# Performance work log

Hardware: AMD Instinct MI355X
Metric: run time of the kernel (lower is better)

Reference implementation:

```python
import jax, jax.numpy as jnp
from jax import lax
import numpy as np

B, P, C = 16, 21824, 2          # batch, num_priors, num_classes
KCAND = 1024                    # candidate cap for jittable NMS
TOP_K = 750
CONF_THRESH = 0.3
IOU_THRESH = 0.01
VAR = (0.1, 0.2)
IMG_SCALE = 1024.0


def setup_inputs() -> dict:
    key = jax.random.key(0)
    k1, k2, k3 = jax.random.split(key, 3)
    return {
        "boxes_logits": jax.random.normal(k1, (B, P, 4), dtype=jnp.float32),
        "cls_logits": jax.random.normal(k2, (B, P, C), dtype=jnp.float32),
        "priors": jax.random.uniform(k3, (P, 4), dtype=jnp.float32),
    }


def decode(loc, priors):
    # priors are (cx, cy, w, h); loc are SSD-style offsets
    xy = priors[..., :2] + loc[..., :2] * VAR[0] * priors[..., 2:]
    wh = priors[..., 2:] * jnp.exp(loc[..., 2:] * VAR[1])
    x1y1 = xy - wh * 0.5
    x2y2 = x1y1 + wh
    return jnp.concatenate([x1y1, x2y2], axis=-1) * IMG_SCALE


def iou_matrix(b):
    # b: [K,4] in x1y1x2y2; torchvision-style IoU (areas unclamped, inter clamped)
    area = (b[:, 2] - b[:, 0]) * (b[:, 3] - b[:, 1])
    lt = jnp.maximum(b[:, None, :2], b[None, :, :2])
    rb = jnp.minimum(b[:, None, 2:], b[None, :, 2:])
    wh = jnp.clip(rb - lt, 0.0)
    inter = wh[..., 0] * wh[..., 1]
    union = area[:, None] + area[None, :] - inter
    return inter / jnp.maximum(union, 1e-9)


def greedy_nms(iou, valid, thresh):
    # boxes assumed sorted by descending score; returns keep mask [K]
    K = iou.shape[0]
    iou = jnp.where(jnp.eye(K, dtype=bool), 0.0, iou)  # ignore self-overlap

    def step(suppressed, i):
        keep_i = jnp.logical_and(~suppressed[i], valid[i])
        suppressed = jnp.logical_or(suppressed, keep_i & (iou[i] > thresh))
        return suppressed, keep_i

    _, keep = lax.scan(step, jnp.zeros(K, dtype=bool), jnp.arange(K))
    return keep


def _detect_one(boxes, scores_all):
    # boxes [P,4], scores_all [P,C]
    scores = scores_all[:, 1:].reshape(-1)                        # drop background
    labels = jnp.broadcast_to(jnp.arange(1, C), (P, C - 1)).reshape(-1)
    bx = jnp.broadcast_to(boxes[:, None, :], (P, C - 1, 4)).reshape(-1, 4)

    masked = jnp.where(scores > CONF_THRESH, scores, -1.0)
    top_scores, idx = lax.top_k(masked, KCAND)                    # score-sorted candidates
    cb = bx[idx]                                                  # [K,4]
    cl = labels[idx]                                              # [K]
    valid = top_scores > CONF_THRESH

    # batched_nms: offset boxes per class so classes never overlap
    max_c = jnp.max(jnp.where(valid[:, None], cb, 0.0))
    off = cl.astype(cb.dtype)[:, None] * (max_c + 1.0)
    keep = greedy_nms(iou_matrix(cb + off), valid, IOU_THRESH)

    kept_scores = jnp.where(keep, top_scores, -1.0)
    final_s, kidx = lax.top_k(kept_scores, TOP_K)                 # keep[:top_k] in score order
    mask = keep[kidx]
    out_boxes = jnp.where(mask[:, None], cb[kidx], 0.0)
    out_scores = jnp.where(mask, final_s, 0.0)
    out_labels = jnp.where(mask, cl[kidx], 0)
    return out_boxes, out_scores, out_labels, mask


def reference(boxes_logits, cls_logits, priors):
    scores_logits = jax.nn.softmax(cls_logits, axis=2)            # [B,P,C]
    boxes = decode(boxes_logits, priors)                          # [B,P,4]
    pred_boxes, pred_scores, pred_labels, mask = jax.vmap(_detect_one)(boxes, scores_logits)
    return pred_boxes, pred_scores, pred_labels, mask
```

## Files before the change

### kernel.cpp

```cpp
#include <hip/hip_runtime.h>

typedef unsigned long long u64;
typedef unsigned int u32;

#define KC 1024
#define TOPK 750
#define CONF 0.3f
#define IOU_T 0.01f
#define WINB 0x2F80u
#define NW 128
#define CCAP 2048

__device__ __forceinline__ u64 score_key(const float* __restrict__ c2, u32 p) {
    float a0 = c2[0], a1 = c2[1];
    float m  = fmaxf(a0, a1);
    float e0 = expf(a0 - m), e1 = expf(a1 - m);
    float s  = e1 / (e0 + e1);
    float ms = s > CONF ? s : -1.0f;
    u32 u = __float_as_uint(ms);
    u32 mapped = (u & 0x80000000u) ? ~u : (u | 0x80000000u);
    return ((u64)mapped << 32) | (u32)(~p);
}

__device__ __forceinline__ void decode_key(u64 key, int b, int tid,
        const float* __restrict__ bl, const float* __restrict__ priors, int P,
        float& x1, float& y1, float& x2, float& y2, float& score, bool& valid) {
    u32 mapped = (u32)(key >> 32);
    u32 fb = (mapped & 0x80000000u) ? (mapped & 0x7fffffffu) : ~mapped;
    float s = __uint_as_float(fb);
    u32 p = ~(u32)(key & 0xffffffffull);
    if (key == 0ull) { s = -1.0f; p = (u32)tid; }
    score = s; valid = (s > CONF);
    const float* pr4 = priors + (size_t)p * 4;
    const float* lc  = bl + ((size_t)b * P + p) * 4;
    float pcx = pr4[0], pcy = pr4[1], pw = pr4[2], ph = pr4[3];
    float lx = lc[0], ly = lc[1], lw = lc[2], lh = lc[3];
    float cx = pcx + lx * 0.1f * pw;
    float cy = pcy + ly * 0.1f * ph;
    float w  = pw * expf(lw * 0.2f);
    float h  = ph * expf(lh * 0.2f);
    float t1x = cx - w * 0.5f;
    float t1y = cy - h * 0.5f;
    x1 = t1x * 1024.0f;
    y1 = t1y * 1024.0f;
    x2 = (t1x + w) * 1024.0f;
    y2 = (t1y + h) * 1024.0f;
}

__global__ __launch_bounds__(1024) void k_hist(const float* __restrict__ cls,
                                               u32* __restrict__ hist, int P) {
    __shared__ u32 lh[NW];
    int t = threadIdx.x;
    if (t < NW) lh[t] = 0;
    __syncthreads();
    int p = blockIdx.x * 1024 + t;
    int b = blockIdx.y;
    if (p < P) {
        u64 k = score_key(cls + ((size_t)b * P + p) * 2, (u32)p);
        u32 wbin = (u32)(k >> 50) - WINB;
        if (wbin < (u32)NW) atomicAdd(&lh[wbin], 1u);
    }
    __syncthreads();
    if (t < NW) { u32 c = lh[t]; if (c) atomicAdd(&hist[(size_t)b * NW + t], c); }
}

__global__ __launch_bounds__(256) void k_compact(const float* __restrict__ cls,
        const u32* __restrict__ hist, u32* __restrict__ sufx, u32* __restrict__ tot,
        u32* __restrict__ bfill, u64* __restrict__ cbuf2, int P) {
    int b = blockIdx.y, t = threadIdx.x;
    __shared__ u32 sh[NW], sa[NW], sb_[NW];
    __shared__ int sh_cut;
    if (t == 0) sh_cut = 0;
    if (t < NW) { u32 h = hist[(size_t)b * NW + t]; sh[t] = h; sa[t] = h; }
    __syncthreads();
    u32 *src = sa, *dst = sb_;
    for (int d = 1; d < NW; d <<= 1) {
        if (t < NW) dst[t] = src[t] + ((t + d < NW) ? src[t + d] : 0u);
        __syncthreads();
        u32* tmp = src; src = dst; dst = tmp;
    }
    if (t < NW && src[t] >= KC) atomicMax(&sh_cut, t);
    __syncthreads();
    int cutw = sh_cut;
    if (blockIdx.x == 0) {
        if (t < NW) sufx[(size_t)b * NW + t] = src[t] - sh[t];
        if (t == 0) tot[b] = src[cutw];
    }
    int p = blockIdx.x * 256 + t;
    if (p < P) {
        u64 k = score_key(cls + ((size_t)b * P + p) * 2, (u32)p);
        u32 wbin = (u32)(k >> 50) - WINB;
        if (wbin < (u32)NW && (int)wbin >= cutw) {
            u32 pos = (src[wbin] - sh[wbin]) + atomicAdd(&bfill[(size_t)b * NW + wbin], 1u);
            if (pos < CCAP) cbuf2[(size_t)b * CCAP + pos] = k;
        }
    }
}

__global__ void k_rank(const u64* __restrict__ cbuf2, const u32* __restrict__ hist,
                       const u32* __restrict__ sufx, const u32* __restrict__ tot,
                       u64* __restrict__ csorted) {
    int b = blockIdx.y;
    u32 s = blockIdx.x * 64 + threadIdx.x;
    u32 T = tot[b]; if (T > CCAP) T = CCAP;
    if (s >= T) return;
    const u64* cb = cbuf2 + (size_t)b * CCAP;
    u64 key = cb[s];
    u32 w = (u32)(key >> 50) - WINB;
    u32 seg0 = sufx[(size_t)b * NW + w];
    u32 segN = seg0 + hist[(size_t)b * NW + w];
    if (segN > T) segN = T;
    u32 cnt = 0;
    for (u32 j = seg0; j < segN; ++j) cnt += (cb[j] > key) ? 1u : 0u;
    u32 r = seg0 + cnt;
    if (r < KC) csorted[(size_t)b * KC + r] = key;
}

__global__ __launch_bounds__(1024) void k_iou(const u64* __restrict__ csorted,
        const float* __restrict__ bl, const float* __restrict__ priors,
        u64* __restrict__ rows, int P) {
    int b = blockIdx.y, tid = threadIdx.x;
    int rowbase = blockIdx.x * 16;
    __shared__ float sx1[KC], sy1[KC], sx2[KC], sy2[KC], sar[KC];
    __shared__ float smax[KC];
    float x1, y1, x2, y2, score; bool valid;
    decode_key(csorted[(size_t)b * KC + tid], b, tid, bl, priors, P,
               x1, y1, x2, y2, score, valid);
    smax[tid] = valid ? fmaxf(fmaxf(x1, y1), fmaxf(x2, y2)) : 0.0f;
    __syncthreads();
    for (int st = 512; st > 0; st >>= 1) {
        if (tid < st) smax[tid] = fmaxf(smax[tid], smax[tid + st]);
        __syncthreads();
    }
    float off = smax[0] + 1.0f;
    float xs1 = x1 + off, ys1 = y1 + off, xs2 = x2 + off, ys2 = y2 + off;
    sx1[tid] = xs1; sy1[tid] = ys1; sx2[tid] = xs2; sy2[tid] = ys2;
    sar[tid] = (xs2 - xs1) * (ys2 - ys1);
    __syncthreads();

    int w = tid >> 6, lane = tid & 63;
    int r = rowbase + w;
    float rx1 = sx1[r], ry1 = sy1[r], rx2 = sx2[r], ry2 = sy2[r], rar = sar[r];
    u64* rb = rows + ((size_t)b * KC + r) * 16;
    #pragma unroll 4
    for (int c = 0; c < 16; ++c) {
        int col = c * 64 + lane;
        float ltx = fmaxf(rx1, sx1[col]), lty = fmaxf(ry1, sy1[col]);
        float rbx = fminf(rx2, sx2[col]), rby = fminf(ry2, sy2[col]);
        float ww = fmaxf(rbx - ltx, 0.0f), hh = fmaxf(rby - lty, 0.0f);
        float inter = ww * hh;
        float uni = rar + sar[col] - inter;
        float iou = inter / fmaxf(uni, 1e-9f);
        bool pred = (iou > IOU_T) && (col != r);
        u64 m = __ballot(pred);
        if (lane == 0) rb[c] = m;
    }
}

__global__ __launch_bounds__(1024) void k_scan(const u64* __restrict__ csorted,
        const u64* __restrict__ rows, const float* __restrict__ bl,
        const float* __restrict__ priors, float* __restrict__ out, int P, int B) {
    int b = blockIdx.x, tid = threadIdx.x;
    __shared__ u64 vw[16], keepw[16];
    float x1, y1, x2, y2, score; bool valid;
    decode_key(csorted[(size_t)b * KC + tid], b, tid, bl, priors, P,
               x1, y1, x2, y2, score, valid);
    u64 bal = __ballot(valid);
    if ((tid & 63) == 0) vw[tid >> 6] = bal;
    __syncthreads();

    if (tid < 16) {
        int lane = tid;
        u64 supp = ~vw[lane];
        u64 kw = 0;
        const u64* rb = rows + (size_t)b * KC * 16;
        for (int w = 0; w < 16; ++w) {
            u64 sw = __shfl(supp, w);
            u64 rem = ~sw;
            while (rem) {
                int bit = __ffsll((long long)rem) - 1;
                int i = w * 64 + bit;
                supp |= rb[(size_t)i * 16 + lane];
                if (lane == w) kw |= 1ull << bit;
                sw = __shfl(supp, w);
                u64 above = (bit == 63) ? 0ull : (~0ull << (bit + 1));
                rem = ~sw & above;
            }
        }
        keepw[lane] = kw;
    }
    __syncthreads();

    int wq = tid >> 6, bq = tid & 63;
    u64 myw = keepw[wq];
    bool kept = (myw >> bq) & 1ull;
    int rank = 0, nk = 0;
    #pragma unroll
    for (int w2 = 0; w2 < 16; ++w2) {
        int pc = __popcll(keepw[w2]);
        nk += pc;
        if (w2 < wq) rank += pc;
    }
    rank += __popcll(myw & ((1ull << bq) - 1ull));

    float* ob  = out;
    float* osc = out + (size_t)B * TOPK * 4;
    float* olb = osc + (size_t)B * TOPK;
    float* omk = olb + (size_t)B * TOPK;

    if (kept && rank < TOPK) {
        size_t o = (size_t)b * TOPK + rank;
        ob[o * 4 + 0] = x1; ob[o * 4 + 1] = y1;
        ob[o * 4 + 2] = x2; ob[o * 4 + 3] = y2;
        osc[o] = score;
        olb[o] = 1.0f;
        omk[o] = 1.0f;
    }
    int zstart = nk < TOPK ? nk : TOPK;
    if (tid >= zstart && tid < TOPK) {
        size_t o = (size_t)b * TOPK + tid;
        ob[o * 4 + 0] = 0.0f; ob[o * 4 + 1] = 0.0f;
        ob[o * 4 + 2] = 0.0f; ob[o * 4 + 3] = 0.0f;
        osc[o] = 0.0f;
        olb[o] = 0.0f;
        omk[o] = 0.0f;
    }
}

extern "C" void kernel_launch(void* const* d_in, const int* in_sizes, int n_in,
                              void* d_out, int out_size, void* d_ws, size_t ws_size,
                              hipStream_t stream) {
    const float* boxes_logits = (const float*)d_in[0];
    const float* cls_logits   = (const float*)d_in[1];
    const float* priors       = (const float*)d_in[2];
    int P = in_sizes[2] / 4;
    int B = in_sizes[0] / (P * 4);
    float* out = (float*)d_out;
    char* wsb = (char*)d_ws;

    size_t HIST_B  = (size_t)B * NW * sizeof(u32);
    size_t BFILL_B = (size_t)B * NW * sizeof(u32);
    size_t CSORT_B = (size_t)B * KC * sizeof(u64);
    size_t SUFX_B  = (size_t)B * NW * sizeof(u32);
    size_t TOT_B   = 256;
    size_t CBUF2_B = (size_t)B * CCAP * sizeof(u64);
    u32* hist    = (u32*)wsb;
    u32* bfill   = (u32*)(wsb + HIST_B);
    u64* csorted = (u64*)(wsb + HIST_B + BFILL_B);
    u32* sufx    = (u32*)(wsb + HIST_B + BFILL_B + CSORT_B);
    u32* tot     = (u32*)(wsb + HIST_B + BFILL_B + CSORT_B + SUFX_B);
    u64* cbuf2   = (u64*)(wsb + HIST_B + BFILL_B + CSORT_B + SUFX_B + TOT_B);
    u64* rows    = (u64*)(wsb + HIST_B + BFILL_B + CSORT_B + SUFX_B + TOT_B + CBUF2_B);

    hipMemsetAsync(wsb, 0, HIST_B + BFILL_B + CSORT_B, stream);

    hipLaunchKernelGGL(k_hist,    dim3((P + 1023) / 1024, B), dim3(1024), 0, stream,
                       cls_logits, hist, P);
    hipLaunchKernelGGL(k_compact, dim3((P + 255) / 256, B),   dim3(256),  0, stream,
                       cls_logits, hist, sufx, tot, bfill, cbuf2, P);
    hipLaunchKernelGGL(k_rank,    dim3(CCAP / 64, B),         dim3(64),   0, stream,
                       cbuf2, hist, sufx, tot, csorted);
    hipLaunchKernelGGL(k_iou,     dim3(KC / 16, B),           dim3(1024), 0, stream,
                       csorted, boxes_logits, priors, rows, P);
    hipLaunchKernelGGL(k_scan,    dim3(B),                    dim3(1024), 0, stream,
                       csorted, rows, boxes_logits, priors, out, P, B);
}
```

Measured before the change: 155.4 us.

## Decode candidate boxes once in rank kernel and widen IoU row tiles

Box decoding (prior and logit gathers plus exp) moves into the rank kernel, which writes each sorted candidate's box to a workspace buffer. The IoU and scan kernels now read those stored boxes instead of decoding them again. Before, every IoU block repeated the decode and the max-reduction for all 1024 candidates. Each IoU block now handles 64 rows instead of 16, so there are a quarter as many blocks doing that shared setup. Slots with no candidate are never written in the box buffer, so their uninitialized contents feed into the IoU bits; this should only affect rows and columns that are never kept.

```diff
diff --git a/kernel.cpp b/kernel.cpp
--- a/kernel.cpp
+++ b/kernel.cpp
@@ -22,31 +22,6 @@
     return ((u64)mapped << 32) | (u32)(~p);
 }
 
-__device__ __forceinline__ void decode_key(u64 key, int b, int tid,
-        const float* __restrict__ bl, const float* __restrict__ priors, int P,
-        float& x1, float& y1, float& x2, float& y2, float& score, bool& valid) {
-    u32 mapped = (u32)(key >> 32);
-    u32 fb = (mapped & 0x80000000u) ? (mapped & 0x7fffffffu) : ~mapped;
-    float s = __uint_as_float(fb);
-    u32 p = ~(u32)(key & 0xffffffffull);
-    if (key == 0ull) { s = -1.0f; p = (u32)tid; }
-    score = s; valid = (s > CONF);
-    const float* pr4 = priors + (size_t)p * 4;
-    const float* lc  = bl + ((size_t)b * P + p) * 4;
-    float pcx = pr4[0], pcy = pr4[1], pw = pr4[2], ph = pr4[3];
-    float lx = lc[0], ly = lc[1], lw = lc[2], lh = lc[3];
-    float cx = pcx + lx * 0.1f * pw;
-    float cy = pcy + ly * 0.1f * ph;
-    float w  = pw * expf(lw * 0.2f);
-    float h  = ph * expf(lh * 0.2f);
-    float t1x = cx - w * 0.5f;
-    float t1y = cy - h * 0.5f;
-    x1 = t1x * 1024.0f;
-    y1 = t1y * 1024.0f;
-    x2 = (t1x + w) * 1024.0f;
-    y2 = (t1y + h) * 1024.0f;
-}
-
 __global__ __launch_bounds__(1024) void k_hist(const float* __restrict__ cls,
                                                u32* __restrict__ hist, int P) {
     __shared__ u32 lh[NW];
@@ -97,9 +72,11 @@
     }
 }
 
-__global__ void k_rank(const u64* __restrict__ cbuf2, const u32* __restrict__ hist,
-                       const u32* __restrict__ sufx, const u32* __restrict__ tot,
-                       u64* __restrict__ csorted) {
+__global__ void k_rankdec(const u64* __restrict__ cbuf2, const u32* __restrict__ hist,
+                          const u32* __restrict__ sufx, const u32* __restrict__ tot,
+                          u64* __restrict__ csorted, float* __restrict__ cboxes,
+                          const float* __restrict__ bl, const float* __restrict__ priors,
+                          int P) {
     int b = blockIdx.y;
     u32 s = blockIdx.x * 64 + threadIdx.x;
     u32 T = tot[b]; if (T > CCAP) T = CCAP;
@@ -113,58 +90,81 @@
     u32 cnt = 0;
     for (u32 j = seg0; j < segN; ++j) cnt += (cb[j] > key) ? 1u : 0u;
     u32 r = seg0 + cnt;
-    if (r < KC) csorted[(size_t)b * KC + r] = key;
+    if (r >= KC) return;
+    csorted[(size_t)b * KC + r] = key;
+
+    u32 p = ~(u32)(key & 0xffffffffull);
+    const float* pr4 = priors + (size_t)p * 4;
+    const float* lc  = bl + ((size_t)b * P + p) * 4;
+    float pcx = pr4[0], pcy = pr4[1], pw = pr4[2], ph = pr4[3];
+    float lx = lc[0], ly = lc[1], lw = lc[2], lh = lc[3];
+    float cx = pcx + lx * 0.1f * pw;
+    float cy = pcy + ly * 0.1f * ph;
+    float ww = pw * expf(lw * 0.2f);
+    float hh = ph * expf(lh * 0.2f);
+    float t1x = cx - ww * 0.5f;
+    float t1y = cy - hh * 0.5f;
+    float4 bx;
+    bx.x = t1x * 1024.0f;
+    bx.y = t1y * 1024.0f;
+    bx.z = (t1x + ww) * 1024.0f;
+    bx.w = (t1y + hh) * 1024.0f;
+    *reinterpret_cast<float4*>(cboxes + ((size_t)b * KC + r) * 4) = bx;
 }
 
 __global__ __launch_bounds__(1024) void k_iou(const u64* __restrict__ csorted,
-        const float* __restrict__ bl, const float* __restrict__ priors,
-        u64* __restrict__ rows, int P) {
+        const float* __restrict__ cboxes, u64* __restrict__ rows) {
     int b = blockIdx.y, tid = threadIdx.x;
-    int rowbase = blockIdx.x * 16;
     __shared__ float sx1[KC], sy1[KC], sx2[KC], sy2[KC], sar[KC];
     __shared__ float smax[KC];
-    float x1, y1, x2, y2, score; bool valid;
-    decode_key(csorted[(size_t)b * KC + tid], b, tid, bl, priors, P,
-               x1, y1, x2, y2, score, valid);
-    smax[tid] = valid ? fmaxf(fmaxf(x1, y1), fmaxf(x2, y2)) : 0.0f;
+    u64 key = csorted[(size_t)b * KC + tid];
+    bool valid = (key != 0ull);
+    float4 bx = reinterpret_cast<const float4*>(cboxes + (size_t)b * KC * 4)[tid];
+    smax[tid] = valid ? fmaxf(fmaxf(bx.x, bx.y), fmaxf(bx.z, bx.w)) : 0.0f;
     __syncthreads();
     for (int st = 512; st > 0; st >>= 1) {
         if (tid < st) smax[tid] = fmaxf(smax[tid], smax[tid + st]);
         __syncthreads();
     }
     float off = smax[0] + 1.0f;
-    float xs1 = x1 + off, ys1 = y1 + off, xs2 = x2 + off, ys2 = y2 + off;
+    float xs1 = bx.x + off, ys1 = bx.y + off, xs2 = bx.z + off, ys2 = bx.w + off;
     sx1[tid] = xs1; sy1[tid] = ys1; sx2[tid] = xs2; sy2[tid] = ys2;
     sar[tid] = (xs2 - xs1) * (ys2 - ys1);
     __syncthreads();
 
     int w = tid >> 6, lane = tid & 63;
-    int r = rowbase + w;
-    float rx1 = sx1[r], ry1 = sy1[r], rx2 = sx2[r], ry2 = sy2[r], rar = sar[r];
-    u64* rb = rows + ((size_t)b * KC + r) * 16;
-    #pragma unroll 4
-    for (int c = 0; c < 16; ++c) {
-        int col = c * 64 + lane;
-        float ltx = fmaxf(rx1, sx1[col]), lty = fmaxf(ry1, sy1[col]);
-        float rbx = fminf(rx2, sx2[col]), rby = fminf(ry2, sy2[col]);
-        float ww = fmaxf(rbx - ltx, 0.0f), hh = fmaxf(rby - lty, 0.0f);
-        float inter = ww * hh;
-        float uni = rar + sar[col] - inter;
-        float iou = inter / fmaxf(uni, 1e-9f);
-        bool pred = (iou > IOU_T) && (col != r);
-        u64 m = __ballot(pred);
-        if (lane == 0) rb[c] = m;
+    u64* rbb = rows + (size_t)b * KC * 16;
+    #pragma unroll
+    for (int rr = 0; rr < 4; ++rr) {
+        int r = blockIdx.x * 64 + w * 4 + rr;
+        float rx1 = sx1[r], ry1 = sy1[r], rx2 = sx2[r], ry2 = sy2[r], rar = sar[r];
+        u64* rb = rbb + (size_t)r * 16;
+        #pragma unroll 4
+        for (int c = 0; c < 16; ++c) {
+            int col = c * 64 + lane;
+            float ltx = fmaxf(rx1, sx1[col]), lty = fmaxf(ry1, sy1[col]);
+            float rbx = fminf(rx2, sx2[col]), rby = fminf(ry2, sy2[col]);
+            float w2 = fmaxf(rbx - ltx, 0.0f), h2 = fmaxf(rby - lty, 0.0f);
+            float inter = w2 * h2;
+            float uni = rar + sar[col] - inter;
+            float iou = inter / fmaxf(uni, 1e-9f);
+            bool pred = (iou > IOU_T) && (col != r);
+            u64 m = __ballot(pred);
+            if (lane == 0) rb[c] = m;
+        }
     }
 }
 
 __global__ __launch_bounds__(1024) void k_scan(const u64* __restrict__ csorted,
-        const u64* __restrict__ rows, const float* __restrict__ bl,
-        const float* __restrict__ priors, float* __restrict__ out, int P, int B) {
+        const u64* __restrict__ rows, const float* __restrict__ cboxes,
+        float* __restrict__ out, int B) {
     int b = blockIdx.x, tid = threadIdx.x;
     __shared__ u64 vw[16], keepw[16];
-    float x1, y1, x2, y2, score; bool valid;
-    decode_key(csorted[(size_t)b * KC + tid], b, tid, bl, priors, P,
-               x1, y1, x2, y2, score, valid);
+    u64 key = csorted[(size_t)b * KC + tid];
+    bool valid = (key != 0ull);
+    u32 mapped = (u32)(key >> 32);
+    u32 fb = (mapped & 0x80000000u) ? (mapped & 0x7fffffffu) : ~mapped;
+    float score = __uint_as_float(fb);
     u64 bal = __ballot(valid);
     if ((tid & 63) == 0) vw[tid >> 6] = bal;
     __syncthreads();
@@ -210,8 +210,8 @@
 
     if (kept && rank < TOPK) {
         size_t o = (size_t)b * TOPK + rank;
-        ob[o * 4 + 0] = x1; ob[o * 4 + 1] = y1;
-        ob[o * 4 + 2] = x2; ob[o * 4 + 3] = y2;
+        float4 bx = reinterpret_cast<const float4*>(cboxes)[(size_t)b * KC + tid];
+        *reinterpret_cast<float4*>(ob + o * 4) = bx;
         osc[o] = score;
         olb[o] = 1.0f;
         omk[o] = 1.0f;
@@ -219,8 +219,8 @@
     int zstart = nk < TOPK ? nk : TOPK;
     if (tid >= zstart && tid < TOPK) {
         size_t o = (size_t)b * TOPK + tid;
-        ob[o * 4 + 0] = 0.0f; ob[o * 4 + 1] = 0.0f;
-        ob[o * 4 + 2] = 0.0f; ob[o * 4 + 3] = 0.0f;
+        float4 z; z.x = z.y = z.z = z.w = 0.0f;
+        *reinterpret_cast<float4*>(ob + o * 4) = z;
         osc[o] = 0.0f;
         olb[o] = 0.0f;
         omk[o] = 0.0f;
@@ -244,13 +244,15 @@
     size_t SUFX_B  = (size_t)B * NW * sizeof(u32);
     size_t TOT_B   = 256;
     size_t CBUF2_B = (size_t)B * CCAP * sizeof(u64);
+    size_t CBOX_B  = (size_t)B * KC * 4 * sizeof(float);
     u32* hist    = (u32*)wsb;
     u32* bfill   = (u32*)(wsb + HIST_B);
     u64* csorted = (u64*)(wsb + HIST_B + BFILL_B);
     u32* sufx    = (u32*)(wsb + HIST_B + BFILL_B + CSORT_B);
     u32* tot     = (u32*)(wsb + HIST_B + BFILL_B + CSORT_B + SUFX_B);
     u64* cbuf2   = (u64*)(wsb + HIST_B + BFILL_B + CSORT_B + SUFX_B + TOT_B);
-    u64* rows    = (u64*)(wsb + HIST_B + BFILL_B + CSORT_B + SUFX_B + TOT_B + CBUF2_B);
+    float* cboxes= (float*)(wsb + HIST_B + BFILL_B + CSORT_B + SUFX_B + TOT_B + CBUF2_B);
+    u64* rows    = (u64*)(wsb + HIST_B + BFILL_B + CSORT_B + SUFX_B + TOT_B + CBUF2_B + CBOX_B);
 
     hipMemsetAsync(wsb, 0, HIST_B + BFILL_B + CSORT_B, stream);
 
@@ -258,10 +260,10 @@
                        cls_logits, hist, P);
     hipLaunchKernelGGL(k_compact, dim3((P + 255) / 256, B),   dim3(256),  0, stream,
                        cls_logits, hist, sufx, tot, bfill, cbuf2, P);
-    hipLaunchKernelGGL(k_rank,    dim3(CCAP / 64, B),         dim3(64),   0, stream,
-                       cbuf2, hist, sufx, tot, csorted);
-    hipLaunchKernelGGL(k_iou,     dim3(KC / 16, B),           dim3(1024), 0, stream,
-                       csorted, boxes_logits, priors, rows, P);
+    hipLaunchKernelGGL(k_rankdec, dim3(CCAP / 64, B),         dim3(64),   0, stream,
+                       cbuf2, hist, sufx, tot, csorted, cboxes, boxes_logits, priors, P);
+    hipLaunchKernelGGL(k_iou,     dim3(KC / 64, B),           dim3(1024), 0, stream,
+                       csorted, cboxes, rows);
     hipLaunchKernelGGL(k_scan,    dim3(B),                    dim3(1024), 0, stream,
-                       csorted, rows, boxes_logits, priors, out, P, B);
-}
+                       csorted, rows, cboxes, out, B);
+}
```

Measured after the change: 154.0 us. Within noise of the previous version (-0.9%).
